# Kernel optimization log

Hardware: AMD Instinct MI355X
Metric: run time of the kernel (lower is better)

Reference implementation:

```python
import jax, jax.numpy as jnp
import numpy as np

SCALE = 480  # matches init scale_factor

def _pchip_slopes(y):
    """Fritsch-Carlson monotone cubic slopes for uniform unit spacing.
    y: [B, T] -> slopes [B, T]. Same math as scipy.interpolate.PchipInterpolator
    with h_i == 1 (t_in = arange(T))."""
    delta = y[:, 1:] - y[:, :-1]            # [B, T-1] secant slopes (h=1)
    d0, d1 = delta[:, :-1], delta[:, 1:]    # [B, T-2]
    prod = d0 * d1
    safe = jnp.where(prod > 0, d0 + d1, 1.0)
    # uniform spacing -> weighted harmonic mean reduces to plain harmonic mean
    interior = jnp.where(prod > 0, 2.0 * prod / safe, 0.0)

    def edge(dA, dB):
        # one-sided three-point estimate, h0 = h1 = 1
        d = (3.0 * dA - dB) * 0.5
        d = jnp.where(jnp.sign(d) != jnp.sign(dA), 0.0, d)
        d = jnp.where((jnp.sign(dA) != jnp.sign(dB)) & (jnp.abs(d) > 3.0 * jnp.abs(dA)),
                      3.0 * dA, d)
        return d

    left = edge(delta[:, 0], delta[:, 1])[:, None]
    right = edge(delta[:, -1], delta[:, -2])[:, None]
    return jnp.concatenate([left, interior, right], axis=1)  # [B, T]

def _pchip_upsample(x, scale):
    B, _, T = x.shape
    y = x[:, 0, :]                           # [B, T]
    d = _pchip_slopes(y)                     # [B, T]
    T_out = T * scale
    # query grid spanning the full knot range t_in = 0..T-1 (intended behavior)
    t = jnp.linspace(0.0, float(T - 1), T_out)
    idx = jnp.clip(jnp.floor(t).astype(jnp.int32), 0, T - 2)  # interval index
    s = t - idx                              # local coordinate in [0, 1]
    one_m_s = 1.0 - s
    s2 = s * s
    h00 = (1.0 + 2.0 * s) * one_m_s * one_m_s
    h10 = s * one_m_s * one_m_s
    h01 = s2 * (3.0 - 2.0 * s)
    h11 = s2 * (s - 1.0)
    # gather + cubic Hermite eval, fully vectorized over [B, T_out]
    out = (h00 * y[:, idx] + h10 * d[:, idx]
           + h01 * y[:, idx + 1] + h11 * d[:, idx + 1])
    return out[:, None, :]                   # [B, 1, T_out]

def setup_inputs() -> dict:
    key = jax.random.key(0)
    x = jax.random.normal(key, (32, 1, 2048), dtype=jnp.float32)
    return {"x": x}

def reference(x):
    return _pchip_upsample(x, SCALE)
```

## Files before the change

### kernel.cpp

```cpp
#include <hip/hip_runtime.h>

#define T_IN 2048
#define UPSCALE 480
#define T_OUT (T_IN * UPSCALE)
#define BPB 64
#define CHUNK (T_OUT / BPB)
#define NTHREADS 256
#define ITERS (CHUNK / 4 / NTHREADS)
#define NINTERVAL (T_IN - 1)

__device__ __forceinline__ float signf(float x) {
    return (x > 0.f) ? 1.f : ((x < 0.f) ? -1.f : 0.f);
}

__device__ __forceinline__ float edge_slope(float dA, float dB) {
    float d = (3.f * dA - dB) * 0.5f;
    if (signf(d) != signf(dA)) {
        d = 0.f;
    } else if ((signf(dA) != signf(dB)) && (fabsf(d) > 3.f * fabsf(dA))) {
        d = 3.f * dA;
    }
    return d;
}

__device__ __forceinline__ float slope_at(const float* sy, int i) {
    if (i == 0) {
        float dA = sy[1] - sy[0];
        float dB = sy[2] - sy[1];
        return edge_slope(dA, dB);
    } else if (i == T_IN - 1) {
        float dA = sy[T_IN - 1] - sy[T_IN - 2];
        float dB = sy[T_IN - 2] - sy[T_IN - 3];
        return edge_slope(dA, dB);
    } else {
        float d0 = sy[i] - sy[i - 1];
        float d1 = sy[i + 1] - sy[i];
        float p = d0 * d1;
        return (p > 0.f) ? (2.f * p / (d0 + d1)) : 0.f;
    }
}

__global__ __launch_bounds__(NTHREADS) void pchip_upsample_kernel(
    const float* __restrict__ x, float* __restrict__ out)
{
    __shared__ float  sy[T_IN];
    __shared__ float4 scoef[NINTERVAL];

    const int b   = blockIdx.y;
    const int cb  = blockIdx.x;
    const int tid = threadIdx.x;

    const float* xb = x + (size_t)b * T_IN;
    for (int i = tid; i < T_IN; i += NTHREADS) sy[i] = xb[i];
    __syncthreads();

    for (int i = tid; i < NINTERVAL; i += NTHREADS) {
        float y0 = sy[i], y1 = sy[i + 1];
        float d0 = slope_at(sy, i);
        float d1 = slope_at(sy, i + 1);
        float dy = y1 - y0;
        float4 c;
        c.x = y0;
        c.y = d0;
        c.z = 3.f * dy - 2.f * d0 - d1;
        c.w = d0 + d1 - 2.f * dy;
        scoef[i] = c;
    }
    __syncthreads();

    const float STEP = (float)(T_IN - 1) / (float)(T_OUT - 1);

    float4* outv = (float4*)(out + (size_t)b * T_OUT + (size_t)cb * CHUNK);
    const int jbase = cb * CHUNK;

    #pragma unroll
    for (int it = 0; it < ITERS; ++it) {
        const int g  = it * NTHREADS + tid;
        const int j0 = jbase + g * 4;
        float4 r;
        #pragma unroll
        for (int k = 0; k < 4; ++k) {
            float t = (float)(j0 + k) * STEP;
            int idx = (int)t;
            idx = idx > (NINTERVAL - 1) ? (NINTERVAL - 1) : idx;
            float s = t - (float)idx;
            float4 c = scoef[idx];
            float v = __builtin_fmaf(__builtin_fmaf(__builtin_fmaf(c.w, s, c.z), s, c.y), s, c.x);
            if (k == 0) r.x = v;
            else if (k == 1) r.y = v;
            else if (k == 2) r.z = v;
            else r.w = v;
        }
        outv[g] = r;
    }
}

extern "C" void kernel_launch(void* const* d_in, const int* in_sizes, int n_in,
                              void* d_out, int out_size, void* d_ws, size_t ws_size,
                              hipStream_t stream) {
    (void)d_ws; (void)ws_size; (void)n_in; (void)out_size;
    const float* x = (const float*)d_in[0];
    float* out = (float*)d_out;
    const int B = in_sizes[0] / T_IN;

    dim3 grid(BPB, B);
    pchip_upsample_kernel<<<grid, NTHREADS, 0, stream>>>(x, out);
}
```

Measured before the change: 29.22 us.

## Compute PCHIP coefficients per output quad from global reads, drop shared-memory setup

```diff
diff --git a/kernel.cpp b/kernel.cpp
--- a/kernel.cpp
+++ b/kernel.cpp
@@ -23,74 +23,63 @@
     return d;
 }
 
-__device__ __forceinline__ float slope_at(const float* sy, int i) {
-    if (i == 0) {
-        float dA = sy[1] - sy[0];
-        float dB = sy[2] - sy[1];
-        return edge_slope(dA, dB);
-    } else if (i == T_IN - 1) {
-        float dA = sy[T_IN - 1] - sy[T_IN - 2];
-        float dB = sy[T_IN - 2] - sy[T_IN - 3];
-        return edge_slope(dA, dB);
-    } else {
-        float d0 = sy[i] - sy[i - 1];
-        float d1 = sy[i + 1] - sy[i];
-        float p = d0 * d1;
-        return (p > 0.f) ? (2.f * p / (d0 + d1)) : 0.f;
-    }
+__device__ __forceinline__ float interior_slope(float dl, float dr) {
+    float p = dl * dr;
+    return (p > 0.f) ? (2.f * p / (dl + dr)) : 0.f;
 }
 
 __global__ __launch_bounds__(NTHREADS) void pchip_upsample_kernel(
     const float* __restrict__ x, float* __restrict__ out)
 {
-    __shared__ float  sy[T_IN];
-    __shared__ float4 scoef[NINTERVAL];
-
     const int b   = blockIdx.y;
     const int cb  = blockIdx.x;
     const int tid = threadIdx.x;
 
-    const float* xb = x + (size_t)b * T_IN;
-    for (int i = tid; i < T_IN; i += NTHREADS) sy[i] = xb[i];
-    __syncthreads();
-
-    for (int i = tid; i < NINTERVAL; i += NTHREADS) {
-        float y0 = sy[i], y1 = sy[i + 1];
-        float d0 = slope_at(sy, i);
-        float d1 = slope_at(sy, i + 1);
-        float dy = y1 - y0;
-        float4 c;
-        c.x = y0;
-        c.y = d0;
-        c.z = 3.f * dy - 2.f * d0 - d1;
-        c.w = d0 + d1 - 2.f * dy;
-        scoef[i] = c;
-    }
-    __syncthreads();
-
     const float STEP = (float)(T_IN - 1) / (float)(T_OUT - 1);
+    const float* __restrict__ y = x + (size_t)b * T_IN;
 
     float4* outv = (float4*)(out + (size_t)b * T_OUT + (size_t)cb * CHUNK);
     const int jbase = cb * CHUNK;
 
-    #pragma unroll
+    #pragma unroll 3
     for (int it = 0; it < ITERS; ++it) {
         const int g  = it * NTHREADS + tid;
         const int j0 = jbase + g * 4;
+
+        float t0 = (float)j0 * STEP;
+        int idx = (int)t0;
+        idx = idx > (NINTERVAL - 1) ? (NINTERVAL - 1) : idx;
+        float s0 = t0 - (float)idx;
+
+        const int im1 = (idx > 0) ? idx - 1 : 0;
+        const int ip2 = (idx < T_IN - 2) ? idx + 2 : T_IN - 1;
+
+        float ym1 = y[im1];
+        float y0  = y[idx];
+        float y1  = y[idx + 1];
+        float y2  = y[ip2];
+
+        float dl = y0 - ym1;
+        float dc = y1 - y0;
+        float dr = y2 - y1;
+
+        float d0 = interior_slope(dl, dc);
+        if (idx == 0) d0 = edge_slope(dc, dr);
+        float d1 = interior_slope(dc, dr);
+        if (idx == NINTERVAL - 1) d1 = edge_slope(dc, dl);
+
+        float c0 = y0;
+        float c1 = d0;
+        float c2 = __builtin_fmaf(3.f, dc, -2.f * d0) - d1;
+        float c3 = (d0 + d1) - 2.f * dc;
+
         float4 r;
-        #pragma unroll
-        for (int k = 0; k < 4; ++k) {
-            float t = (float)(j0 + k) * STEP;
-            int idx = (int)t;
-            idx = idx > (NINTERVAL - 1) ? (NINTERVAL - 1) : idx;
-            float s = t - (float)idx;
-            float4 c = scoef[idx];
-            float v = __builtin_fmaf(__builtin_fmaf(__builtin_fmaf(c.w, s, c.z), s, c.y), s, c.x);
-            if (k == 0) r.x = v;
-            else if (k == 1) r.y = v;
-            else if (k == 2) r.z = v;
-            else r.w = v;
-        }
+        float s = s0;
+        r.x = __builtin_fmaf(__builtin_fmaf(__builtin_fmaf(c3, s, c2), s, c1), s, c0); s += STEP;
+        r.y = __builtin_fmaf(__builtin_fmaf(__builtin_fmaf(c3, s, c2), s, c1), s, c0); s += STEP;
+        r.z = __builtin_fmaf(__builtin_fmaf(__builtin_fmaf(c3, s, c2), s, c1), s, c0); s += STEP;
+        r.w = __builtin_fmaf(__builtin_fmaf(__builtin_fmaf(c3, s, c2), s, c1), s, c0);
+
         outv[g] = r;
     }
 }
```

New measurement: 25.78 us. -11.8%, faster.
